# Kernel tuning notes

Measured on AMD Instinct MI355X. Metric: run time of the kernel, lower is better.

Reference implementation:

```python
import jax, jax.numpy as jnp
import numpy as np

BLOCK_SIZE = 64
B, H, S, D = 2, 16, 2048, 64


def _make_mask(seq_len: int, bs: int):
    # Vectorized equivalent of the torch loop:
    # M[i,j] = True iff (i and j in same block) or (j is a block-head column).
    idx = jnp.arange(seq_len)
    blk = idx // bs
    same_block = blk[:, None] == blk[None, :]           # (S, S)
    head_col = ((idx % bs) == 0)[None, :]               # (1, S)
    return same_block | head_col                         # (S, S) bool


def setup_inputs() -> dict:
    key = jax.random.key(0)
    kq, kk, kv = jax.random.split(key, 3)
    Q = jax.random.normal(kq, (B, H, S, D), dtype=jnp.float32)
    K = jax.random.normal(kk, (B, H, S, D), dtype=jnp.float32)
    V = jax.random.normal(kv, (B, H, S, D), dtype=jnp.float32)
    return {"Q": Q, "K": K, "V": V}


def reference(Q, K, V):
    b, h, s, d = Q.shape
    M = _make_mask(s, BLOCK_SIZE)                        # (S, S) bool
    scores = jnp.einsum('bhsd,bhtd->bhst', Q, K) / jnp.sqrt(jnp.asarray(d, Q.dtype))
    # Faithful to the original: masked_fill where M is True (fills the
    # 'allowed' positions with -inf, as the torch source does).
    neg_inf = jnp.asarray(-jnp.inf, scores.dtype)
    scores = jnp.where(M[None, None, :, :], neg_inf, scores)
    attn = jax.nn.softmax(scores, axis=-1)               # (B, H, S, S)
    out = jnp.einsum('bhst,bhtd->bhsd', attn, V)         # (B, H, S, D)
    return (out, attn, M)
```

## Files before the change

### kernel.cpp

```cpp
#include <hip/hip_runtime.h>
#include <hip/hip_bf16.h>
#include <cmath>

#define S_LEN 2048
#define D_DIM 64
#define BM 128
#define BN 64
#define NKT 32
#define NBH 32
#define NRT (S_LEN / BM)
#define LDPF 68
#define LDP 72

typedef float f32x4 __attribute__((ext_vector_type(4)));
typedef short s16x8 __attribute__((ext_vector_type(8)));
typedef unsigned int u32x4 __attribute__((ext_vector_type(4)));

union PFU { u32x4 u; s16x8 s; };

__device__ __forceinline__ unsigned short f2b(float x) {
  union { float f; unsigned int u; } un; un.f = x;
  unsigned int u = un.u;
  unsigned int r = (u + 0x7FFF + ((u >> 16) & 1)) >> 16;
  return (unsigned short)r;
}

__device__ __forceinline__ unsigned int fbits(float x) {
  union { float f; unsigned int u; } un; un.f = x; return un.u;
}

__device__ __forceinline__ unsigned int pk2(float lo, float hi) {
  return __builtin_amdgcn_perm(fbits(hi), fbits(lo), 0x07060302u);
}

__device__ __forceinline__ s16x8 pack8(float4 a, float4 b) {
  s16x8 r;
  r[0] = (short)f2b(a.x); r[1] = (short)f2b(a.y);
  r[2] = (short)f2b(a.z); r[3] = (short)f2b(a.w);
  r[4] = (short)f2b(b.x); r[5] = (short)f2b(b.y);
  r[6] = (short)f2b(b.z); r[7] = (short)f2b(b.w);
  return r;
}

typedef __attribute__((address_space(1))) const unsigned int GU32;
typedef __attribute__((address_space(3))) unsigned int LU32;
__device__ __forceinline__ void gload16(const void* g, void* l) {
  __builtin_amdgcn_global_load_lds((GU32*)g, (LU32*)l, 16, 0, 0);
}

__global__ __launch_bounds__(256) void cvt_kernel(
    const float* __restrict__ in, unsigned short* __restrict__ out) {
  size_t off = ((size_t)blockIdx.x * 256 + threadIdx.x) * 8;
  float4 a = *(const float4*)(in + off);
  float4 b = *(const float4*)(in + off + 4);
  *(s16x8*)(out + off) = pack8(a, b);
}

__global__ __launch_bounds__(256) void vtr_kernel(
    const float* __restrict__ V, unsigned short* __restrict__ Vt) {
  __shared__ unsigned short L[64 * 72];
  const int tid = threadIdx.x;
  const int bh = blockIdx.y;
  const int s0 = blockIdx.x * 64;
  const float* Vp = V + ((size_t)bh * S_LEN + s0) * D_DIM;
  for (int it = 0; it < 4; ++it) {
    int lin = it * 256 + tid;
    int r = lin >> 4;
    int c = (lin & 15) << 2;
    float4 v = *(const float4*)(Vp + (size_t)r * D_DIM + c);
    L[(c + 0) * 72 + r] = f2b(v.x);
    L[(c + 1) * 72 + r] = f2b(v.y);
    L[(c + 2) * 72 + r] = f2b(v.z);
    L[(c + 3) * 72 + r] = f2b(v.w);
  }
  __syncthreads();
  unsigned short* Vo = Vt + (size_t)bh * D_DIM * S_LEN + s0;
  for (int it = 0; it < 2; ++it) {
    int lin = it * 256 + tid;
    int d = lin >> 3;
    int c8 = (lin & 7) * 8;
    s16x8 v = *(const s16x8*)&L[d * 72 + c8];
    *(s16x8*)(Vo + (size_t)d * S_LEN + c8) = v;
  }
}

__global__ __launch_bounds__(512, 4) void bsattn_fast(
    const float* __restrict__ Qg_, const unsigned short* __restrict__ Kb,
    const unsigned short* __restrict__ Vtb, float* __restrict__ outg,
    float* __restrict__ attng) {
  __shared__ __align__(16) unsigned short Kl[2][64 * 64];
  __shared__ __align__(16) unsigned short Vl[2][64 * 64];
  __shared__ __align__(16) float Pl[BM * LDPF];

  const int tid = threadIdx.x;
  const int w  = tid >> 6;
  const int l  = tid & 63;
  const int lr = l & 15;
  const int lh = l >> 4;

  const int lin = blockIdx.x;
  const int xcd = lin & 7;
  const int ix  = lin >> 3;
  const int bh  = xcd + 8 * (ix >> 4);
  const int rt  = ix & 15;
  const int row0 = rt * BM;
  const int mb  = rt * 2 + (w >> 2);

  const unsigned short* Kh = Kb  + (size_t)bh * S_LEN * D_DIM;
  const unsigned short* Vh = Vtb + (size_t)bh * D_DIM * S_LEN;
  float* outp  = outg  + (size_t)bh * S_LEN * D_DIM;
  float* attnp = attng + (size_t)bh * S_LEN * S_LEN;

  const float* Qrow = Qg_ + ((size_t)bh * S_LEN + row0 + w * 16 + lr) * D_DIM;
  const s16x8 qf0 = pack8(*(const float4*)(Qrow + lh * 8),
                          *(const float4*)(Qrow + lh * 8 + 4));
  const s16x8 qf1 = pack8(*(const float4*)(Qrow + 32 + lh * 8),
                          *(const float4*)(Qrow + 32 + lh * 8 + 4));

  const float C = 0.18033688011112042f;

  auto STAGE_K = [&](int kt, int b) {
    int row = tid >> 3;
    int c = (tid & 7) ^ (row & 7);
    gload16(Kh + (size_t)kt * 4096 + row * 64 + c * 8, &Kl[b][tid * 8]);
  };
  auto STAGE_V = [&](int kt, int b) {
    int row = tid >> 3;
    int c = (tid & 7) ^ (row & 7);
    gload16(Vh + (size_t)row * S_LEN + kt * 64 + c * 8, &Vl[b][tid * 8]);
  };

  auto QKACC = [&](int b, f32x4* acc) {
#pragma unroll
    for (int j16 = 0; j16 < 4; ++j16) {
      const int j = j16 * 16 + lr;
      const int sw = (j & 7) * 8;
      const s16x8 kf0 = *(const s16x8*)&Kl[b][j * 64 + ((lh * 8) ^ sw)];
      const s16x8 kf1 = *(const s16x8*)&Kl[b][j * 64 + ((32 + lh * 8) ^ sw)];
      f32x4 a = {0.f, 0.f, 0.f, 0.f};
      a = __builtin_amdgcn_mfma_f32_16x16x32_bf16(qf0, kf0, a, 0, 0, 0);
      a = __builtin_amdgcn_mfma_f32_16x16x32_bf16(qf1, kf1, a, 0, 0, 0);
      acc[j16] = a;
    }
  };

  auto ATTN_STORE = [&](int kt) {
#pragma unroll
    for (int it = 0; it < 4; ++it) {
      const int arow = w * 16 + it * 4 + lh;
      const f32x4 v = *(const f32x4*)&Pl[arow * LDPF + lr * 4];
      __builtin_nontemporal_store(
          v, (f32x4*)(attnp + (size_t)(row0 + arow) * S_LEN + kt * BN + lr * 4));
    }
  };

  float l_run[4] = {0.f, 0.f, 0.f, 0.f};
  STAGE_K(0, 0);
  __syncthreads();
  for (int kt = 0; kt < NKT; ++kt) {
    const int b = kt & 1;
    if (kt < NKT - 1) STAGE_K(kt + 1, b ^ 1);
    f32x4 acc[4];
    QKACC(b, acc);
    const float ts = (kt == mb) ? 0.f : 1.f;
#pragma unroll
    for (int r = 0; r < 4; ++r) {
      float e0 = __builtin_amdgcn_exp2f(acc[0][r] * C);
      if (lr == 0) e0 = 0.f;
      float e1 = __builtin_amdgcn_exp2f(acc[1][r] * C);
      float e2 = __builtin_amdgcn_exp2f(acc[2][r] * C);
      float e3 = __builtin_amdgcn_exp2f(acc[3][r] * C);
      l_run[r] += ts * (e0 + e1 + e2 + e3);
    }
    __syncthreads();
  }

  STAGE_K(0, 0);
  STAGE_V(0, 0);
#pragma unroll
  for (int off = 8; off >= 1; off >>= 1)
#pragma unroll
    for (int r = 0; r < 4; ++r) l_run[r] += __shfl_xor(l_run[r], off);
  float invl[4];
#pragma unroll
  for (int r = 0; r < 4; ++r) invl[r] = 1.0f / l_run[r];
  __syncthreads();

  f32x4 oacc[4];
#pragma unroll
  for (int d16 = 0; d16 < 4; ++d16) oacc[d16] = (f32x4){0.f, 0.f, 0.f, 0.f};

  for (int kt = 0; kt < NKT; ++kt) {
    const int b = kt & 1;
    if (kt < NKT - 1) { STAGE_K(kt + 1, b ^ 1); STAGE_V(kt + 1, b ^ 1); }
    if (kt > 0) ATTN_STORE(kt - 1);

    f32x4 acc[4];
    QKACC(b, acc);
    const float ts = (kt == mb) ? 0.f : 1.f;
#pragma unroll
    for (int j16 = 0; j16 < 4; ++j16)
#pragma unroll
      for (int r = 0; r < 4; ++r) {
        float e = __builtin_amdgcn_exp2f(acc[j16][r] * C) * ts * invl[r];
        if (j16 == 0 && lr == 0) e = 0.f;
        Pl[(w * 16 + lh * 4 + r) * LDPF + j16 * 16 + lr] = e;
      }

#pragma unroll
    for (int ks = 0; ks < 2; ++ks) {
      const float* prow = &Pl[(w * 16 + lr) * LDPF + ks * 32 + lh * 8];
      float4 pa = *(const float4*)prow;
      float4 pb = *(const float4*)(prow + 4);
      PFU p;
      p.u = (u32x4){pk2(pa.x, pa.y), pk2(pa.z, pa.w),
                    pk2(pb.x, pb.y), pk2(pb.z, pb.w)};
#pragma unroll
      for (int d16 = 0; d16 < 4; ++d16) {
        const int vr = d16 * 16 + lr;
        const s16x8 vf = *(const s16x8*)
            &Vl[b][vr * 64 + ((ks * 32 + lh * 8) ^ ((vr & 7) * 8))];
        oacc[d16] = __builtin_amdgcn_mfma_f32_16x16x32_bf16(p.s, vf, oacc[d16], 0, 0, 0);
      }
    }

    __builtin_amdgcn_sched_barrier(0);
    if (kt == 0) {
      asm volatile("s_waitcnt vmcnt(0)" ::: "memory");
    } else {
      asm volatile("s_waitcnt vmcnt(4)" ::: "memory");
    }
    __builtin_amdgcn_s_barrier();
    __builtin_amdgcn_sched_barrier(0);
  }
  ATTN_STORE(NKT - 1);

#pragma unroll
  for (int d16 = 0; d16 < 4; ++d16)
#pragma unroll
    for (int r = 0; r < 4; ++r) {
      int irow = w * 16 + lh * 4 + r;
      __builtin_nontemporal_store(
          oacc[d16][r], outp + (size_t)(row0 + irow) * D_DIM + d16 * 16 + lr);
    }
}

__global__ __launch_bounds__(256) void bsattn_kernel(
    const float* __restrict__ Qg_, const float* __restrict__ Kg_,
    const float* __restrict__ Vg_, float* __restrict__ outg,
    float* __restrict__ attng) {
  __shared__ __align__(16) unsigned short Ql[64 * LDP];
  __shared__ __align__(16) unsigned short Kl[64 * LDP];
  __shared__ __align__(16) unsigned short Vt[64 * LDP];
  __shared__ __align__(16) unsigned short Pp[64 * LDP];
  const int tid = threadIdx.x;
  const int w  = tid >> 6;
  const int l  = tid & 63;
  const int lr = l & 15;
  const int lh = l >> 4;
  const int rt = blockIdx.x;
  const int bh = blockIdx.y;
  const int row0 = rt * 64;
  const float* Qg = Qg_ + (size_t)bh * S_LEN * D_DIM;
  const float* Kg = Kg_ + (size_t)bh * S_LEN * D_DIM;
  const float* Vg = Vg_ + (size_t)bh * S_LEN * D_DIM;
  float* outp  = outg  + (size_t)bh * S_LEN * D_DIM;
  float* attnp = attng + (size_t)bh * S_LEN * S_LEN;
  for (int it = 0; it < 4; ++it) {
    int lin2 = it * 256 + tid;
    int r = lin2 >> 4;
    int c = (lin2 & 15) << 2;
    const float4 v = *(const float4*)(Qg + (size_t)(row0 + r) * D_DIM + c);
    ushort4 bb; bb.x = f2b(v.x); bb.y = f2b(v.y); bb.z = f2b(v.z); bb.w = f2b(v.w);
    *(ushort4*)&Ql[r * LDP + c] = bb;
  }
  __syncthreads();
  const s16x8 qf0 = *(const s16x8*)&Ql[(w * 16 + lr) * LDP + lh * 8];
  const s16x8 qf1 = *(const s16x8*)&Ql[(w * 16 + lr) * LDP + 32 + lh * 8];
  float m_run[4] = {-1e30f, -1e30f, -1e30f, -1e30f};
  float l_run[4] = {0.f, 0.f, 0.f, 0.f};
  for (int kt = 0; kt < NKT; ++kt) {
    if (kt == rt) continue;
    __syncthreads();
    const float* Kt = Kg + (size_t)kt * BN * D_DIM;
    for (int it = 0; it < 4; ++it) {
      int lin2 = it * 256 + tid;
      int r = lin2 >> 4;
      int c = (lin2 & 15) << 2;
      const float4 v = *(const float4*)(Kt + r * D_DIM + c);
      ushort4 bb; bb.x = f2b(v.x); bb.y = f2b(v.y); bb.z = f2b(v.z); bb.w = f2b(v.w);
      *(ushort4*)&Kl[r * LDP + c] = bb;
    }
    __syncthreads();
    f32x4 acc[4];
#pragma unroll
    for (int j16 = 0; j16 < 4; ++j16) {
      f32x4 a = {0.f, 0.f, 0.f, 0.f};
      s16x8 kf0 = *(const s16x8*)&Kl[(j16 * 16 + lr) * LDP + lh * 8];
      a = __builtin_amdgcn_mfma_f32_16x16x32_bf16(qf0, kf0, a, 0, 0, 0);
      s16x8 kf1 = *(const s16x8*)&Kl[(j16 * 16 + lr) * LDP + 32 + lh * 8];
      a = __builtin_amdgcn_mfma_f32_16x16x32_bf16(qf1, kf1, a, 0, 0, 0);
      acc[j16] = a;
    }
#pragma unroll
    for (int r = 0; r < 4; ++r) {
      float s0 = acc[0][r] * 0.125f;
      if (lr == 0) s0 = -INFINITY;
      float s1 = acc[1][r] * 0.125f;
      float s2 = acc[2][r] * 0.125f;
      float s3 = acc[3][r] * 0.125f;
      float tm = fmaxf(fmaxf(s0, s1), fmaxf(s2, s3));
      float mn = fmaxf(m_run[r], tm);
      float sc = __expf(m_run[r] - mn);
      l_run[r] = l_run[r] * sc + __expf(s0 - mn) + __expf(s1 - mn) +
                 __expf(s2 - mn) + __expf(s3 - mn);
      m_run[r] = mn;
    }
  }
#pragma unroll
  for (int off = 8; off >= 1; off >>= 1) {
#pragma unroll
    for (int r = 0; r < 4; ++r) {
      float mo = __shfl_xor(m_run[r], off);
      float lo = __shfl_xor(l_run[r], off);
      float mn = fmaxf(m_run[r], mo);
      l_run[r] = l_run[r] * __expf(m_run[r] - mn) + lo * __expf(mo - mn);
      m_run[r] = mn;
    }
  }
  float invl[4];
#pragma unroll
  for (int r = 0; r < 4; ++r) invl[r] = 1.0f / l_run[r];
  f32x4 oacc[4];
#pragma unroll
  for (int d16 = 0; d16 < 4; ++d16) oacc[d16] = (f32x4){0.f, 0.f, 0.f, 0.f};
  for (int kt = 0; kt < NKT; ++kt) {
    if (kt == rt) {
      for (int it = 0; it < 4; ++it) {
        int lin2 = it * 256 + tid;
        int r = lin2 >> 4;
        int c = (lin2 & 15) << 2;
        float4 z = {0.f, 0.f, 0.f, 0.f};
        *(float4*)(attnp + (size_t)(row0 + r) * S_LEN + kt * BN + c) = z;
      }
      continue;
    }
    __syncthreads();
    const float* Kt  = Kg + (size_t)kt * BN * D_DIM;
    const float* Vtg = Vg + (size_t)kt * BN * D_DIM;
    for (int it = 0; it < 4; ++it) {
      int lin2 = it * 256 + tid;
      int r = lin2 >> 4;
      int c = (lin2 & 15) << 2;
      const float4 v = *(const float4*)(Kt + r * D_DIM + c);
      ushort4 bb; bb.x = f2b(v.x); bb.y = f2b(v.y); bb.z = f2b(v.z); bb.w = f2b(v.w);
      *(ushort4*)&Kl[r * LDP + c] = bb;
      const float4 vv = *(const float4*)(Vtg + r * D_DIM + c);
      Vt[(c + 0) * LDP + r] = f2b(vv.x);
      Vt[(c + 1) * LDP + r] = f2b(vv.y);
      Vt[(c + 2) * LDP + r] = f2b(vv.z);
      Vt[(c + 3) * LDP + r] = f2b(vv.w);
    }
    __syncthreads();
    f32x4 acc[4];
#pragma unroll
    for (int j16 = 0; j16 < 4; ++j16) {
      f32x4 a = {0.f, 0.f, 0.f, 0.f};
      s16x8 kf0 = *(const s16x8*)&Kl[(j16 * 16 + lr) * LDP + lh * 8];
      a = __builtin_amdgcn_mfma_f32_16x16x32_bf16(qf0, kf0, a, 0, 0, 0);
      s16x8 kf1 = *(const s16x8*)&Kl[(j16 * 16 + lr) * LDP + 32 + lh * 8];
      a = __builtin_amdgcn_mfma_f32_16x16x32_bf16(qf1, kf1, a, 0, 0, 0);
      acc[j16] = a;
    }
#pragma unroll
    for (int j16 = 0; j16 < 4; ++j16) {
#pragma unroll
      for (int r = 0; r < 4; ++r) {
        float s = acc[j16][r] * 0.125f;
        if (j16 == 0 && lr == 0) s = -INFINITY;
        int irow = w * 16 + lh * 4 + r;
        float p = __expf(s - m_run[r]) * invl[r];
        attnp[(size_t)(row0 + irow) * S_LEN + kt * BN + j16 * 16 + lr] = p;
        Pp[irow * LDP + j16 * 16 + lr] = f2b(p);
      }
    }
    __syncthreads();
#pragma unroll
    for (int ks = 0; ks < 2; ++ks) {
      s16x8 pf = *(const s16x8*)&Pp[(w * 16 + lr) * LDP + ks * 32 + lh * 8];
#pragma unroll
      for (int d16 = 0; d16 < 4; ++d16) {
        s16x8 vf = *(const s16x8*)&Vt[(d16 * 16 + lr) * LDP + ks * 32 + lh * 8];
        oacc[d16] = __builtin_amdgcn_mfma_f32_16x16x32_bf16(pf, vf, oacc[d16], 0, 0, 0);
      }
    }
  }
#pragma unroll
  for (int d16 = 0; d16 < 4; ++d16) {
#pragma unroll
    for (int r = 0; r < 4; ++r) {
      int irow = w * 16 + lh * 4 + r;
      outp[(size_t)(row0 + irow) * D_DIM + d16 * 16 + lr] = oacc[d16][r];
    }
  }
}

__global__ __launch_bounds__(256) void mask_kernel(float* __restrict__ M) {
  int idx = blockIdx.x * 256 + threadIdx.x;
  int i  = idx >> 9;
  int c4 = (idx & 511) << 2;
  int iblk = i >> 6;
  int jblk = c4 >> 6;
  bool same = (jblk == iblk);
  f32x4 v;
  v[0] = (same || ((c4 & 63) == 0)) ? 1.f : 0.f;
  v[1] = same ? 1.f : 0.f;
  v[2] = same ? 1.f : 0.f;
  v[3] = same ? 1.f : 0.f;
  __builtin_nontemporal_store(v, (f32x4*)(M + (size_t)idx * 4));
}

extern "C" void kernel_launch(void* const* d_in, const int* in_sizes, int n_in,
                              void* d_out, int out_size, void* d_ws, size_t ws_size,
                              hipStream_t stream) {
  const float* Q = (const float*)d_in[0];
  const float* K = (const float*)d_in[1];
  const float* V = (const float*)d_in[2];
  float* out  = (float*)d_out;
  float* attn = out + (size_t)NBH * S_LEN * D_DIM;
  float* M    = attn + (size_t)NBH * S_LEN * S_LEN;

  const size_t elems = (size_t)NBH * S_LEN * D_DIM;
  const size_t need  = elems * 2 * 2;

  if (ws_size >= need) {
    unsigned short* Kb  = (unsigned short*)d_ws;
    unsigned short* Vtb = Kb + elems;
    cvt_kernel<<<(int)(elems / 8 / 256), 256, 0, stream>>>(K, Kb);
    vtr_kernel<<<dim3(S_LEN / 64, NBH), 256, 0, stream>>>(V, Vtb);
    bsattn_fast<<<NBH * NRT, 512, 0, stream>>>(Q, Kb, Vtb, out, attn);
  } else {
    dim3 grid(S_LEN / 64, NBH);
    bsattn_kernel<<<grid, 256, 0, stream>>>(Q, K, V, out, attn);
  }
  mask_kernel<<<(S_LEN * S_LEN / 4) / 256, 256, 0, stream>>>(M);
}
```

Measured before the change: 158.7 us.

## Split denominator pass into separate kernel, fuse K/V prep and mask write

Merges the K conversion and V transpose kernels into one prep kernel. Moves the softmax-denominator pass out of the attention kernel into its own kernel, which uses a 4-deep K LDS pipeline with explicit waitcnt/barriers, writes inverse row sums to workspace, and also emits the mask rows. The main attention kernel then reads the precomputed inverse denominators. This cuts launches and lets the denominator pass use a deeper prefetch, at the cost of an extra workspace round trip and the denom kernel reading Q and K a second time.

```diff
diff --git a/kernel.cpp b/kernel.cpp
--- a/kernel.cpp
+++ b/kernel.cpp
@@ -48,20 +48,24 @@
   __builtin_amdgcn_global_load_lds((GU32*)g, (LU32*)l, 16, 0, 0);
 }
 
-__global__ __launch_bounds__(256) void cvt_kernel(
-    const float* __restrict__ in, unsigned short* __restrict__ out) {
-  size_t off = ((size_t)blockIdx.x * 256 + threadIdx.x) * 8;
-  float4 a = *(const float4*)(in + off);
-  float4 b = *(const float4*)(in + off + 4);
-  *(s16x8*)(out + off) = pack8(a, b);
-}
-
-__global__ __launch_bounds__(256) void vtr_kernel(
-    const float* __restrict__ V, unsigned short* __restrict__ Vt) {
+__global__ __launch_bounds__(256) void prep_kernel(
+    const float* __restrict__ K, const float* __restrict__ V,
+    unsigned short* __restrict__ Kb, unsigned short* __restrict__ Vt) {
   __shared__ unsigned short L[64 * 72];
   const int tid = threadIdx.x;
   const int bh = blockIdx.y;
   const int s0 = blockIdx.x * 64;
+
+  const float* Kp = K + ((size_t)bh * S_LEN + s0) * D_DIM;
+  unsigned short* Ko = Kb + ((size_t)bh * S_LEN + s0) * D_DIM;
+#pragma unroll
+  for (int it = 0; it < 2; ++it) {
+    int off = tid * 8 + it * 2048;
+    float4 a = *(const float4*)(Kp + off);
+    float4 b = *(const float4*)(Kp + off + 4);
+    *(s16x8*)(Ko + off) = pack8(a, b);
+  }
+
   const float* Vp = V + ((size_t)bh * S_LEN + s0) * D_DIM;
   for (int it = 0; it < 4; ++it) {
     int lin = it * 256 + tid;
@@ -84,13 +88,10 @@
   }
 }
 
-__global__ __launch_bounds__(512, 4) void bsattn_fast(
+__global__ __launch_bounds__(512, 4) void denom_kernel(
     const float* __restrict__ Qg_, const unsigned short* __restrict__ Kb,
-    const unsigned short* __restrict__ Vtb, float* __restrict__ outg,
-    float* __restrict__ attng) {
-  __shared__ __align__(16) unsigned short Kl[2][64 * 64];
-  __shared__ __align__(16) unsigned short Vl[2][64 * 64];
-  __shared__ __align__(16) float Pl[BM * LDPF];
+    float* __restrict__ invl_ws, float* __restrict__ Mg) {
+  __shared__ __align__(16) unsigned short Kl[4][64 * 64];
 
   const int tid = threadIdx.x;
   const int w  = tid >> 6;
@@ -106,10 +107,7 @@
   const int row0 = rt * BM;
   const int mb  = rt * 2 + (w >> 2);
 
-  const unsigned short* Kh = Kb  + (size_t)bh * S_LEN * D_DIM;
-  const unsigned short* Vh = Vtb + (size_t)bh * D_DIM * S_LEN;
-  float* outp  = outg  + (size_t)bh * S_LEN * D_DIM;
-  float* attnp = attng + (size_t)bh * S_LEN * S_LEN;
+  const unsigned short* Kh = Kb + (size_t)bh * S_LEN * D_DIM;
 
   const float* Qrow = Qg_ + ((size_t)bh * S_LEN + row0 + w * 16 + lr) * D_DIM;
   const s16x8 qf0 = pack8(*(const float4*)(Qrow + lh * 8),
@@ -118,6 +116,118 @@
                           *(const float4*)(Qrow + 32 + lh * 8 + 4));
 
   const float C = 0.18033688011112042f;
+
+  auto STAGE_K = [&](int kt, int b) {
+    int row = tid >> 3;
+    int c = (tid & 7) ^ (row & 7);
+    gload16(Kh + (size_t)kt * 4096 + row * 64 + c * 8, &Kl[b][tid * 8]);
+  };
+  auto QKACC = [&](int b, f32x4* acc) {
+#pragma unroll
+    for (int j16 = 0; j16 < 4; ++j16) {
+      const int j = j16 * 16 + lr;
+      const int sw = (j & 7) * 8;
+      const s16x8 kf0 = *(const s16x8*)&Kl[b][j * 64 + ((lh * 8) ^ sw)];
+      const s16x8 kf1 = *(const s16x8*)&Kl[b][j * 64 + ((32 + lh * 8) ^ sw)];
+      f32x4 a = {0.f, 0.f, 0.f, 0.f};
+      a = __builtin_amdgcn_mfma_f32_16x16x32_bf16(qf0, kf0, a, 0, 0, 0);
+      a = __builtin_amdgcn_mfma_f32_16x16x32_bf16(qf1, kf1, a, 0, 0, 0);
+      acc[j16] = a;
+    }
+  };
+
+  float l_run[4] = {0.f, 0.f, 0.f, 0.f};
+  STAGE_K(0, 0); STAGE_K(1, 1); STAGE_K(2, 2);
+  asm volatile("s_waitcnt vmcnt(2)" ::: "memory");
+  __builtin_amdgcn_s_barrier();
+  __builtin_amdgcn_sched_barrier(0);
+
+  for (int kt = 0; kt < NKT; ++kt) {
+    STAGE_K((kt + 3) & 31, (kt + 3) & 3);
+    f32x4 acc[4];
+    QKACC(kt & 3, acc);
+    const float ts = (kt == mb) ? 0.f : 1.f;
+#pragma unroll
+    for (int r = 0; r < 4; ++r) {
+      float e0 = __builtin_amdgcn_exp2f(acc[0][r] * C);
+      if (lr == 0) e0 = 0.f;
+      float e1 = __builtin_amdgcn_exp2f(acc[1][r] * C);
+      float e2 = __builtin_amdgcn_exp2f(acc[2][r] * C);
+      float e3 = __builtin_amdgcn_exp2f(acc[3][r] * C);
+      l_run[r] += ts * (e0 + e1 + e2 + e3);
+    }
+    __builtin_amdgcn_sched_barrier(0);
+    asm volatile("s_waitcnt vmcnt(2)" ::: "memory");
+    __builtin_amdgcn_s_barrier();
+    __builtin_amdgcn_sched_barrier(0);
+  }
+
+#pragma unroll
+  for (int off = 8; off >= 1; off >>= 1)
+#pragma unroll
+    for (int r = 0; r < 4; ++r) l_run[r] += __shfl_xor(l_run[r], off);
+
+  if (lr == 0) {
+#pragma unroll
+    for (int r = 0; r < 4; ++r)
+      invl_ws[(size_t)bh * S_LEN + row0 + w * 16 + lh * 4 + r] = 1.0f / l_run[r];
+  }
+
+  {
+    const int i0 = blockIdx.x * 4;
+#pragma unroll
+    for (int rr = 0; rr < 4; ++rr) {
+      const int i = i0 + rr;
+      const int iblk = i >> 6;
+      const int c0 = tid * 4;
+      f32x4 v;
+#pragma unroll
+      for (int c = 0; c < 4; ++c) {
+        const int j = c0 + c;
+        v[c] = ((j >> 6) == iblk) || ((j & 63) == 0) ? 1.f : 0.f;
+      }
+      __builtin_nontemporal_store(v, (f32x4*)(Mg + (size_t)i * S_LEN + c0));
+    }
+  }
+}
+
+__global__ __launch_bounds__(512, 4) void bsattn_fast(
+    const float* __restrict__ Qg_, const unsigned short* __restrict__ Kb,
+    const unsigned short* __restrict__ Vtb, const float* __restrict__ invl_ws,
+    float* __restrict__ outg, float* __restrict__ attng) {
+  __shared__ __align__(16) unsigned short Kl[2][64 * 64];
+  __shared__ __align__(16) unsigned short Vl[2][64 * 64];
+  __shared__ __align__(16) float Pl[BM * LDPF];
+
+  const int tid = threadIdx.x;
+  const int w  = tid >> 6;
+  const int l  = tid & 63;
+  const int lr = l & 15;
+  const int lh = l >> 4;
+
+  const int lin = blockIdx.x;
+  const int xcd = lin & 7;
+  const int ix  = lin >> 3;
+  const int bh  = xcd + 8 * (ix >> 4);
+  const int rt  = ix & 15;
+  const int row0 = rt * BM;
+  const int mb  = rt * 2 + (w >> 2);
+
+  const unsigned short* Kh = Kb  + (size_t)bh * S_LEN * D_DIM;
+  const unsigned short* Vh = Vtb + (size_t)bh * D_DIM * S_LEN;
+  float* outp  = outg  + (size_t)bh * S_LEN * D_DIM;
+  float* attnp = attng + (size_t)bh * S_LEN * S_LEN;
+
+  const float* Qrow = Qg_ + ((size_t)bh * S_LEN + row0 + w * 16 + lr) * D_DIM;
+  const s16x8 qf0 = pack8(*(const float4*)(Qrow + lh * 8),
+                          *(const float4*)(Qrow + lh * 8 + 4));
+  const s16x8 qf1 = pack8(*(const float4*)(Qrow + 32 + lh * 8),
+                          *(const float4*)(Qrow + 32 + lh * 8 + 4));
+
+  const float C = 0.18033688011112042f;
+
+  const float4 iv4 = *(const float4*)(invl_ws + (size_t)bh * S_LEN + row0 + w * 16 + lh * 4);
+  const float invl[4] = {iv4.x, iv4.y, iv4.z, iv4.w};
 
   auto STAGE_K = [&](int kt, int b) {
     int row = tid >> 3;
@@ -129,7 +239,6 @@
     int c = (tid & 7) ^ (row & 7);
     gload16(Vh + (size_t)row * S_LEN + kt * 64 + c * 8, &Vl[b][tid * 8]);
   };
-
   auto QKACC = [&](int b, f32x4* acc) {
 #pragma unroll
     for (int j16 = 0; j16 < 4; ++j16) {
@@ -143,7 +252,6 @@
       acc[j16] = a;
     }
   };
-
   auto ATTN_STORE = [&](int kt) {
 #pragma unroll
     for (int it = 0; it < 4; ++it) {
@@ -154,36 +262,8 @@
     }
   };
 
-  float l_run[4] = {0.f, 0.f, 0.f, 0.f};
-  STAGE_K(0, 0);
-  __syncthreads();
-  for (int kt = 0; kt < NKT; ++kt) {
-    const int b = kt & 1;
-    if (kt < NKT - 1) STAGE_K(kt + 1, b ^ 1);
-    f32x4 acc[4];
-    QKACC(b, acc);
-    const float ts = (kt == mb) ? 0.f : 1.f;
-#pragma unroll
-    for (int r = 0; r < 4; ++r) {
-      float e0 = __builtin_amdgcn_exp2f(acc[0][r] * C);
-      if (lr == 0) e0 = 0.f;
-      float e1 = __builtin_amdgcn_exp2f(acc[1][r] * C);
-      float e2 = __builtin_amdgcn_exp2f(acc[2][r] * C);
-      float e3 = __builtin_amdgcn_exp2f(acc[3][r] * C);
-      l_run[r] += ts * (e0 + e1 + e2 + e3);
-    }
-    __syncthreads();
-  }
-
   STAGE_K(0, 0);
   STAGE_V(0, 0);
-#pragma unroll
-  for (int off = 8; off >= 1; off >>= 1)
-#pragma unroll
-    for (int r = 0; r < 4; ++r) l_run[r] += __shfl_xor(l_run[r], off);
-  float invl[4];
-#pragma unroll
-  for (int r = 0; r < 4; ++r) invl[r] = 1.0f / l_run[r];
   __syncthreads();
 
   f32x4 oacc[4];
@@ -431,17 +511,18 @@
   float* M    = attn + (size_t)NBH * S_LEN * S_LEN;
 
   const size_t elems = (size_t)NBH * S_LEN * D_DIM;
-  const size_t need  = elems * 2 * 2;
+  const size_t need  = elems * 2 * 2 + (size_t)NBH * S_LEN * 4;
 
   if (ws_size >= need) {
     unsigned short* Kb  = (unsigned short*)d_ws;
     unsigned short* Vtb = Kb + elems;
-    cvt_kernel<<<(int)(elems / 8 / 256), 256, 0, stream>>>(K, Kb);
-    vtr_kernel<<<dim3(S_LEN / 64, NBH), 256, 0, stream>>>(V, Vtb);
-    bsattn_fast<<<NBH * NRT, 512, 0, stream>>>(Q, Kb, Vtb, out, attn);
+    float* invl_ws = (float*)(Vtb + elems);
+    prep_kernel<<<dim3(S_LEN / 64, NBH), 256, 0, stream>>>(K, V, Kb, Vtb);
+    denom_kernel<<<NBH * NRT, 512, 0, stream>>>(Q, Kb, invl_ws, M);
+    bsattn_fast<<<NBH * NRT, 512, 0, stream>>>(Q, Kb, Vtb, invl_ws, out, attn);
   } else {
     dim3 grid(S_LEN / 64, NBH);
     bsattn_kernel<<<grid, 256, 0, stream>>>(Q, K, V, out, attn);
-  }
-  mask_kernel<<<(S_LEN * S_LEN / 4) / 256, 256, 0, stream>>>(M);
-}
+    mask_kernel<<<(S_LEN * S_LEN / 4) / 256, 256, 0, stream>>>(M);
+  }
+}
```

After: 166.4 us. 4.8% more time.

## Fuse K/V prep and mask write into attention, store attn directly from MFMA

Applied to the files above, without the earlier changes.

Merges the K convert and V transpose kernels into one prep kernel, and folds the mask write into the attention kernel so two launches go away. The QK MFMA operands are swapped so each lane holds a row segment, which lets the probabilities go straight from registers to global memory and into a bf16 P buffer in LDS instead of round-tripping through a float LDS tile. The first pass gains a 4-deep K prefetch ring that reuses the same LDS stages. This removes launch overhead and LDS traffic, at the cost of more complex buffer indexing and the mask store now sharing bandwidth with the attention kernel.

```diff
diff --git a/kernel.cpp b/kernel.cpp
--- a/kernel.cpp
+++ b/kernel.cpp
@@ -9,14 +9,12 @@
 #define NKT 32
 #define NBH 32
 #define NRT (S_LEN / BM)
-#define LDPF 68
+#define PSTR 72
 #define LDP 72
 
 typedef float f32x4 __attribute__((ext_vector_type(4)));
 typedef short s16x8 __attribute__((ext_vector_type(8)));
-typedef unsigned int u32x4 __attribute__((ext_vector_type(4)));
-
-union PFU { u32x4 u; s16x8 s; };
+typedef unsigned int u32x2 __attribute__((ext_vector_type(2)));
 
 __device__ __forceinline__ unsigned short f2b(float x) {
   union { float f; unsigned int u; } un; un.f = x;
@@ -48,20 +46,24 @@
   __builtin_amdgcn_global_load_lds((GU32*)g, (LU32*)l, 16, 0, 0);
 }
 
-__global__ __launch_bounds__(256) void cvt_kernel(
-    const float* __restrict__ in, unsigned short* __restrict__ out) {
-  size_t off = ((size_t)blockIdx.x * 256 + threadIdx.x) * 8;
-  float4 a = *(const float4*)(in + off);
-  float4 b = *(const float4*)(in + off + 4);
-  *(s16x8*)(out + off) = pack8(a, b);
-}
-
-__global__ __launch_bounds__(256) void vtr_kernel(
-    const float* __restrict__ V, unsigned short* __restrict__ Vt) {
+__global__ __launch_bounds__(256) void prep_kernel(
+    const float* __restrict__ K, const float* __restrict__ V,
+    unsigned short* __restrict__ Kb, unsigned short* __restrict__ Vt) {
   __shared__ unsigned short L[64 * 72];
   const int tid = threadIdx.x;
   const int bh = blockIdx.y;
   const int s0 = blockIdx.x * 64;
+
+  const float* Kp = K + ((size_t)bh * S_LEN + s0) * D_DIM;
+  unsigned short* Ko = Kb + ((size_t)bh * S_LEN + s0) * D_DIM;
+#pragma unroll
+  for (int it = 0; it < 2; ++it) {
+    int off = tid * 8 + it * 2048;
+    float4 a = *(const float4*)(Kp + off);
+    float4 b = *(const float4*)(Kp + off + 4);
+    *(s16x8*)(Ko + off) = pack8(a, b);
+  }
+
   const float* Vp = V + ((size_t)bh * S_LEN + s0) * D_DIM;
   for (int it = 0; it < 4; ++it) {
     int lin = it * 256 + tid;
@@ -87,10 +89,9 @@
 __global__ __launch_bounds__(512, 4) void bsattn_fast(
     const float* __restrict__ Qg_, const unsigned short* __restrict__ Kb,
     const unsigned short* __restrict__ Vtb, float* __restrict__ outg,
-    float* __restrict__ attng) {
-  __shared__ __align__(16) unsigned short Kl[2][64 * 64];
-  __shared__ __align__(16) unsigned short Vl[2][64 * 64];
-  __shared__ __align__(16) float Pl[BM * LDPF];
+    float* __restrict__ attng, float* __restrict__ Mg) {
+  __shared__ __align__(16) unsigned short Stage[4][64 * 64];
+  __shared__ __align__(16) unsigned short Pb[BM * PSTR];
 
   const int tid = threadIdx.x;
   const int w  = tid >> 6;
@@ -122,12 +123,12 @@
   auto STAGE_K = [&](int kt, int b) {
     int row = tid >> 3;
     int c = (tid & 7) ^ (row & 7);
-    gload16(Kh + (size_t)kt * 4096 + row * 64 + c * 8, &Kl[b][tid * 8]);
+    gload16(Kh + (size_t)kt * 4096 + row * 64 + c * 8, &Stage[b][tid * 8]);
   };
   auto STAGE_V = [&](int kt, int b) {
     int row = tid >> 3;
     int c = (tid & 7) ^ (row & 7);
-    gload16(Vh + (size_t)row * S_LEN + kt * 64 + c * 8, &Vl[b][tid * 8]);
+    gload16(Vh + (size_t)row * S_LEN + kt * 64 + c * 8, &Stage[b][tid * 8]);
   };
 
   auto QKACC = [&](int b, f32x4* acc) {
@@ -135,105 +136,114 @@
     for (int j16 = 0; j16 < 4; ++j16) {
       const int j = j16 * 16 + lr;
       const int sw = (j & 7) * 8;
-      const s16x8 kf0 = *(const s16x8*)&Kl[b][j * 64 + ((lh * 8) ^ sw)];
-      const s16x8 kf1 = *(const s16x8*)&Kl[b][j * 64 + ((32 + lh * 8) ^ sw)];
+      const s16x8 kf0 = *(const s16x8*)&Stage[b][j * 64 + ((lh * 8) ^ sw)];
+      const s16x8 kf1 = *(const s16x8*)&Stage[b][j * 64 + ((32 + lh * 8) ^ sw)];
       f32x4 a = {0.f, 0.f, 0.f, 0.f};
-      a = __builtin_amdgcn_mfma_f32_16x16x32_bf16(qf0, kf0, a, 0, 0, 0);
-      a = __builtin_amdgcn_mfma_f32_16x16x32_bf16(qf1, kf1, a, 0, 0, 0);
+      a = __builtin_amdgcn_mfma_f32_16x16x32_bf16(kf0, qf0, a, 0, 0, 0);
+      a = __builtin_amdgcn_mfma_f32_16x16x32_bf16(kf1, qf1, a, 0, 0, 0);
       acc[j16] = a;
     }
   };
 
-  auto ATTN_STORE = [&](int kt) {
-#pragma unroll
-    for (int it = 0; it < 4; ++it) {
-      const int arow = w * 16 + it * 4 + lh;
-      const f32x4 v = *(const f32x4*)&Pl[arow * LDPF + lr * 4];
-      __builtin_nontemporal_store(
-          v, (f32x4*)(attnp + (size_t)(row0 + arow) * S_LEN + kt * BN + lr * 4));
-    }
-  };
-
-  float l_run[4] = {0.f, 0.f, 0.f, 0.f};
-  STAGE_K(0, 0);
+  float l_run = 0.f;
+  STAGE_K(0, 0); STAGE_K(1, 1); STAGE_K(2, 2);
+  asm volatile("s_waitcnt vmcnt(2)" ::: "memory");
+  __builtin_amdgcn_s_barrier();
+  __builtin_amdgcn_sched_barrier(0);
+
+  for (int kt = 0; kt < NKT; ++kt) {
+    STAGE_K((kt + 3) & 31, (kt + 3) & 3);
+    f32x4 acc[4];
+    QKACC(kt & 3, acc);
+    const float ts = (kt == mb) ? 0.f : 1.f;
+    float s = 0.f;
+#pragma unroll
+    for (int j16 = 0; j16 < 4; ++j16)
+#pragma unroll
+      for (int r = 0; r < 4; ++r) {
+        float e = __builtin_amdgcn_exp2f(acc[j16][r] * C);
+        if (j16 == 0 && r == 0 && lh == 0) e = 0.f;
+        s += e;
+      }
+    l_run += ts * s;
+    __builtin_amdgcn_sched_barrier(0);
+    asm volatile("s_waitcnt vmcnt(2)" ::: "memory");
+    __builtin_amdgcn_s_barrier();
+    __builtin_amdgcn_sched_barrier(0);
+  }
+
+  asm volatile("s_waitcnt vmcnt(0)" ::: "memory");
+
+  l_run += __shfl_xor(l_run, 16);
+  l_run += __shfl_xor(l_run, 32);
+  const float invl = 1.0f / l_run;
+
+  {
+    const int i0 = blockIdx.x * 4;
+#pragma unroll
+    for (int rr = 0; rr < 4; ++rr) {
+      const int i = i0 + rr;
+      const int iblk = i >> 6;
+      const int c0 = tid * 4;
+      f32x4 v;
+#pragma unroll
+      for (int c = 0; c < 4; ++c) {
+        const int j = c0 + c;
+        v[c] = ((j >> 6) == iblk) || ((j & 63) == 0) ? 1.f : 0.f;
+      }
+      __builtin_nontemporal_store(v, (f32x4*)(Mg + (size_t)i * S_LEN + c0));
+    }
+  }
+
+  STAGE_V(0, 2);
   __syncthreads();
+
+  f32x4 oacc[4];
+#pragma unroll
+  for (int d16 = 0; d16 < 4; ++d16) oacc[d16] = (f32x4){0.f, 0.f, 0.f, 0.f};
+
+  float* arow_base = attnp + (size_t)(row0 + w * 16 + lr) * S_LEN + lh * 4;
+  unsigned short* prow = &Pb[(w * 16 + lr) * PSTR];
+
   for (int kt = 0; kt < NKT; ++kt) {
-    const int b = kt & 1;
-    if (kt < NKT - 1) STAGE_K(kt + 1, b ^ 1);
+    const int kb = kt & 1;
+    const int vb = 2 + (kt & 1);
+    if (kt < NKT - 1) { STAGE_K(kt + 1, (kt + 1) & 1); STAGE_V(kt + 1, 2 + ((kt + 1) & 1)); }
+
     f32x4 acc[4];
-    QKACC(b, acc);
-    const float ts = (kt == mb) ? 0.f : 1.f;
-#pragma unroll
-    for (int r = 0; r < 4; ++r) {
-      float e0 = __builtin_amdgcn_exp2f(acc[0][r] * C);
-      if (lr == 0) e0 = 0.f;
-      float e1 = __builtin_amdgcn_exp2f(acc[1][r] * C);
-      float e2 = __builtin_amdgcn_exp2f(acc[2][r] * C);
-      float e3 = __builtin_amdgcn_exp2f(acc[3][r] * C);
-      l_run[r] += ts * (e0 + e1 + e2 + e3);
-    }
-    __syncthreads();
-  }
-
-  STAGE_K(0, 0);
-  STAGE_V(0, 0);
-#pragma unroll
-  for (int off = 8; off >= 1; off >>= 1)
-#pragma unroll
-    for (int r = 0; r < 4; ++r) l_run[r] += __shfl_xor(l_run[r], off);
-  float invl[4];
-#pragma unroll
-  for (int r = 0; r < 4; ++r) invl[r] = 1.0f / l_run[r];
-  __syncthreads();
-
-  f32x4 oacc[4];
-#pragma unroll
-  for (int d16 = 0; d16 < 4; ++d16) oacc[d16] = (f32x4){0.f, 0.f, 0.f, 0.f};
-
-  for (int kt = 0; kt < NKT; ++kt) {
-    const int b = kt & 1;
-    if (kt < NKT - 1) { STAGE_K(kt + 1, b ^ 1); STAGE_V(kt + 1, b ^ 1); }
-    if (kt > 0) ATTN_STORE(kt - 1);
-
-    f32x4 acc[4];
-    QKACC(b, acc);
-    const float ts = (kt == mb) ? 0.f : 1.f;
-#pragma unroll
-    for (int j16 = 0; j16 < 4; ++j16)
-#pragma unroll
-      for (int r = 0; r < 4; ++r) {
-        float e = __builtin_amdgcn_exp2f(acc[j16][r] * C) * ts * invl[r];
-        if (j16 == 0 && lr == 0) e = 0.f;
-        Pl[(w * 16 + lh * 4 + r) * LDPF + j16 * 16 + lr] = e;
-      }
+    QKACC(kb, acc);
+    const float sc = ((kt == mb) ? 0.f : 1.f) * invl;
+
+#pragma unroll
+    for (int j16 = 0; j16 < 4; ++j16) {
+      float e0 = __builtin_amdgcn_exp2f(acc[j16][0] * C) * sc;
+      float e1 = __builtin_amdgcn_exp2f(acc[j16][1] * C) * sc;
+      float e2 = __builtin_amdgcn_exp2f(acc[j16][2] * C) * sc;
+      float e3 = __builtin_amdgcn_exp2f(acc[j16][3] * C) * sc;
+      if (j16 == 0 && lh == 0) e0 = 0.f;
+      f32x4 ev = {e0, e1, e2, e3};
+      __builtin_nontemporal_store(ev, (f32x4*)(arow_base + kt * BN + j16 * 16));
+      u32x2 up = {pk2(e0, e1), pk2(e2, e3)};
+      *(u32x2*)(prow + j16 * 16 + lh * 4) = up;
+    }
 
 #pragma unroll
     for (int ks = 0; ks < 2; ++ks) {
-      const float* prow = &Pl[(w * 16 + lr) * LDPF + ks * 32 + lh * 8];
-      float4 pa = *(const float4*)prow;
-      float4 pb = *(const float4*)(prow + 4);
-      PFU p;
-      p.u = (u32x4){pk2(pa.x, pa.y), pk2(pa.z, pa.w),
-                    pk2(pb.x, pb.y), pk2(pb.z, pb.w)};
+      const s16x8 pf = *(const s16x8*)(prow + ks * 32 + lh * 8);
 #pragma unroll
       for (int d16 = 0; d16 < 4; ++d16) {
         const int vr = d16 * 16 + lr;
         const s16x8 vf = *(const s16x8*)
-            &Vl[b][vr * 64 + ((ks * 32 + lh * 8) ^ ((vr & 7) * 8))];
-        oacc[d16] = __builtin_amdgcn_mfma_f32_16x16x32_bf16(p.s, vf, oacc[d16], 0, 0, 0);
+            &Stage[vb][vr * 64 + ((ks * 32 + lh * 8) ^ ((vr & 7) * 8))];
+        oacc[d16] = __builtin_amdgcn_mfma_f32_16x16x32_bf16(pf, vf, oacc[d16], 0, 0, 0);
       }
     }
 
     __builtin_amdgcn_sched_barrier(0);
-    if (kt == 0) {
-      asm volatile("s_waitcnt vmcnt(0)" ::: "memory");
-    } else {
-      asm volatile("s_waitcnt vmcnt(4)" ::: "memory");
-    }
+    asm volatile("s_waitcnt vmcnt(4)" ::: "memory");
     __builtin_amdgcn_s_barrier();
     __builtin_amdgcn_sched_barrier(0);
   }
-  ATTN_STORE(NKT - 1);
 
 #pragma unroll
   for (int d16 = 0; d16 < 4; ++d16)
@@ -311,8 +321,8 @@
       float s3 = acc[3][r] * 0.125f;
       float tm = fmaxf(fmaxf(s0, s1), fmaxf(s2, s3));
       float mn = fmaxf(m_run[r], tm);
-      float sc = __expf(m_run[r] - mn);
-      l_run[r] = l_run[r] * sc + __expf(s0 - mn) + __expf(s1 - mn) +
+      float scx = __expf(m_run[r] - mn);
+      l_run[r] = l_run[r] * scx + __expf(s0 - mn) + __expf(s1 - mn) +
                  __expf(s2 - mn) + __expf(s3 - mn);
       m_run[r] = mn;
     }
@@ -436,12 +446,11 @@
   if (ws_size >= need) {
     unsigned short* Kb  = (unsigned short*)d_ws;
     unsigned short* Vtb = Kb + elems;
-    cvt_kernel<<<(int)(elems / 8 / 256), 256, 0, stream>>>(K, Kb);
-    vtr_kernel<<<dim3(S_LEN / 64, NBH), 256, 0, stream>>>(V, Vtb);
-    bsattn_fast<<<NBH * NRT, 512, 0, stream>>>(Q, Kb, Vtb, out, attn);
+    prep_kernel<<<dim3(S_LEN / 64, NBH), 256, 0, stream>>>(K, V, Kb, Vtb);
+    bsattn_fast<<<NBH * NRT, 512, 0, stream>>>(Q, Kb, Vtb, out, attn, M);
   } else {
     dim3 grid(S_LEN / 64, NBH);
     bsattn_kernel<<<grid, 256, 0, stream>>>(Q, K, V, out, attn);
-  }
-  mask_kernel<<<(S_LEN * S_LEN / 4) / 256, 256, 0, stream>>>(M);
-}
+    mask_kernel<<<(S_LEN * S_LEN / 4) / 256, 256, 0, stream>>>(M);
+  }
+}
```

Measured after the change: 224.1 us. 1.41x slower.
